# Optimization experiments

Hardware: AMD Instinct MI355X
Metric: run time of the kernel (lower is better)

The kernel has to match this reference:

```python
import jax, jax.numpy as jnp
import numpy as np

B, C, S, D = 16, 32, 64, 512
DFF, E = 2048, 8


def setup_inputs() -> dict:
    key = jax.random.key(0)
    ks = jax.random.split(key, 16)
    std = 0.02
    return {
        'x': jax.random.normal(ks[0], (B, C, S, D), jnp.float32),
        'baseline': jax.random.normal(ks[1], (B, C, S, D), jnp.float32),
        'attnres': jax.random.normal(ks[2], (B, C, S, D), jnp.float32),
        'shared_w1': jax.random.normal(ks[3], (DFF, D), jnp.float32) * std,
        'shared_b1': jnp.zeros((DFF,), jnp.float32),
        'shared_w2': jax.random.normal(ks[4], (D, DFF), jnp.float32) * std,
        'shared_b2': jnp.zeros((D,), jnp.float32),
        'spa_router_w': jax.random.normal(ks[5], (E, 3 * D), jnp.float32) * std,
        'spa_router_b': jnp.zeros((E,), jnp.float32),
        'spe_router_w': jax.random.normal(ks[6], (E, 3 * D), jnp.float32) * std,
        'spe_router_b': jnp.zeros((E,), jnp.float32),
        'spa_w1': jax.random.normal(ks[7], (E, DFF, D), jnp.float32) * std,
        'spa_b1': jnp.zeros((E, DFF), jnp.float32),
        'spa_w2': jax.random.normal(ks[8], (E, D, DFF), jnp.float32) * std,
        'spa_b2': jnp.zeros((E, D), jnp.float32),
        'spe_w1': jax.random.normal(ks[9], (E, DFF, D), jnp.float32) * std,
        'spe_b1': jnp.zeros((E, DFF), jnp.float32),
        'spe_w2': jax.random.normal(ks[10], (E, D, DFF), jnp.float32) * std,
        'spe_b2': jnp.zeros((E, D), jnp.float32),
    }


def _route(feat, rw, rb):
    # feat [B, 3D] -> top-1 expert index [B] and its softmax gate weight [B]
    logits = feat @ rw.T + rb            # [B, E]
    p = jax.nn.softmax(logits, axis=-1)
    idx = jnp.argmax(logits, axis=-1)    # [B]
    w = jnp.take_along_axis(p, idx[:, None], axis=-1)[:, 0]
    return idx, w


def _specialist(xf, idx, w1, b1, w2, b2):
    # xf [B, T, D]; per-sample gather of expert weights then batched FFN
    W1, B1 = w1[idx], b1[idx]            # [B, DFF, D], [B, DFF]
    W2, B2 = w2[idx], b2[idx]            # [B, D, DFF], [B, D]
    h = jax.nn.gelu(jnp.einsum('btd,bfd->btf', xf, W1) + B1[:, None, :])
    return jnp.einsum('btf,bdf->btd', h, W2) + B2[:, None, :]


def reference(x, baseline, attnres, shared_w1, shared_b1, shared_w2, shared_b2,
              spa_router_w, spa_router_b, spe_router_w, spe_router_b,
              spa_w1, spa_b1, spa_w2, spa_b2, spe_w1, spe_b1, spe_w2, spe_b2):
    b, d = x.shape[0], x.shape[-1]
    xf = x.reshape(b, -1, d)  # [B, T, D]
    # sample-level AttnRes router features: [B, 3*d_model]
    feat = jnp.concatenate([
        baseline.mean(axis=(1, 2)),
        attnres.mean(axis=(1, 2)),
        (attnres - baseline).mean(axis=(1, 2)),
    ], axis=-1)
    spa_idx, spa_w = _route(feat, spa_router_w, spa_router_b)
    spe_idx, spe_w = _route(feat, spe_router_w, spe_router_b)
    # shared dense FFN (dropout=0 eval)
    shared = jax.nn.gelu(xf @ shared_w1.T + shared_b1) @ shared_w2.T + shared_b2
    spa_out = _specialist(xf, spa_idx, spa_w1, spa_b1, spa_w2, spa_b2)
    spe_out = _specialist(xf, spe_idx, spe_w1, spe_b1, spe_w2, spe_b2)
    y = shared + spa_w[:, None, None] * spa_out + spe_w[:, None, None] * spe_out
    return y.reshape(x.shape)
```

## Files before the change

### kernel.cpp

```cpp
#include <hip/hip_runtime.h>
#include <cstdint>
#include <cstddef>

#define DEV __device__ __forceinline__

typedef unsigned short u16;
typedef _Float16 f16x8 __attribute__((ext_vector_type(8)));
typedef float f32x4 __attribute__((ext_vector_type(4)));

static constexpr int NB  = 16;
static constexpr int T   = 2048;
static constexpr int D   = 512;
static constexpr int DFF = 2048;
static constexpr int NE  = 8;
static constexpr int FEAT = 3 * D;

#define MFMA16 __builtin_amdgcn_mfma_f32_16x16x32_f16

DEV u16 f2h(float f) {
  _Float16 h = (_Float16)f;
  union { _Float16 h; u16 u; } cv; cv.h = h; return cv.u;
}

DEV float gelu_fast(float x) {
  const float t = x * x;
  const float p = x * fmaf(t, -0.07135481627f, -1.59576912161f);
  return __fdividef(x, 1.0f + __expf(p));
}


__global__ void k_part(const float* __restrict__ base, const float* __restrict__ attn,
                       float* __restrict__ part) {
  const int b = blockIdx.x >> 4, ch = blockIdx.x & 15;
  const int d = threadIdx.x;
  const size_t o = ((size_t)b * T + (size_t)ch * 128) * D + d;
  const float* pb = base + o;
  const float* pa = attn + o;
  float sb = 0.f, sa = 0.f;
  for (int r = 0; r < 128; ++r) { sb += pb[(size_t)r * D]; sa += pa[(size_t)r * D]; }
  part[(b * 16 + ch) * D + d] = sb;
  part[NB * 16 * D + (b * 16 + ch) * D + d] = sa;
}

__global__ void k_feat(const float* __restrict__ part, float* __restrict__ feat) {
  const int b = blockIdx.x, d = threadIdx.x;
  float sb = 0.f, sa = 0.f;
  for (int ch = 0; ch < 16; ++ch) {
    sb += part[(b * 16 + ch) * D + d];
    sa += part[NB * 16 * D + (b * 16 + ch) * D + d];
  }
  sb *= (1.0f / 2048.0f); sa *= (1.0f / 2048.0f);
  feat[b * FEAT + d] = sb;
  feat[b * FEAT + D + d] = sa;
  feat[b * FEAT + 2 * D + d] = sa - sb;
}

__global__ void k_zero(int* __restrict__ used) {
  used[threadIdx.x] = 0;
}

__global__ void k_route(const float* __restrict__ feat,
                        const float* __restrict__ rw0, const float* __restrict__ rb0,
                        const float* __restrict__ rw1, const float* __restrict__ rb1,
                        int* __restrict__ idx, float* __restrict__ gate,
                        int* __restrict__ used) {
  const int r = blockIdx.x >> 4, b = blockIdx.x & 15;
  const float* rw = (r == 0) ? rw0 : rw1;
  const float* rb = (r == 0) ? rb0 : rb1;
  const int l = threadIdx.x;
  float p[8];
#pragma unroll
  for (int e = 0; e < 8; ++e) p[e] = 0.f;
  const float* f = feat + b * FEAT;
  for (int k = l; k < FEAT; k += 64) {
    const float fv = f[k];
#pragma unroll
    for (int e = 0; e < 8; ++e) p[e] += fv * rw[e * FEAT + k];
  }
#pragma unroll
  for (int off = 32; off >= 1; off >>= 1) {
#pragma unroll
    for (int e = 0; e < 8; ++e) p[e] += __shfl_xor(p[e], off);
  }
  if (l == 0) {
    float best = -1e30f; int bi = 0;
    float lg[8];
#pragma unroll
    for (int e = 0; e < 8; ++e) {
      lg[e] = p[e] + rb[e];
      if (lg[e] > best) { best = lg[e]; bi = e; }
    }
    float s = 0.f;
#pragma unroll
    for (int e = 0; e < 8; ++e) s += expf(lg[e] - best);
    idx[r * 16 + b] = bi;
    gate[r * 16 + b] = 1.0f / s;
    atomicOr(&used[r * 8 + bi], 1);
  }
}

__global__ void k_btot(const float* __restrict__ b2s, const float* __restrict__ b2a,
                       const float* __restrict__ b2e, const int* __restrict__ idx,
                       const float* __restrict__ gate, float* __restrict__ btot) {
  const int b = blockIdx.x, d = threadIdx.x;
  const int ia = idx[b], ie = idx[16 + b];
  const float ga = gate[b], ge = gate[16 + b];
  btot[b * D + d] = b2s[d] + ga * b2a[ia * D + d] + ge * b2e[ie * D + d];
}

__global__ void k_cast(const float* __restrict__ s, u16* __restrict__ d, long n) {
  const long i = ((long)blockIdx.x * blockDim.x + threadIdx.x) * 4;
  if (i >= n) return;
  const float4 v = *(const float4*)(s + i);
  const unsigned int lo = (unsigned int)f2h(v.x) | ((unsigned int)f2h(v.y) << 16);
  const unsigned int hi = (unsigned int)f2h(v.z) | ((unsigned int)f2h(v.w) << 16);
  *(uint2*)(d + i) = make_uint2(lo, hi);
}

__global__ void k_cast_gated(const float* __restrict__ s, u16* __restrict__ d,
                             const int* __restrict__ used) {
  const int e = blockIdx.x >> 10;
  if (!used[e]) return;
  const long i = (long)e * (DFF * D) + ((long)(blockIdx.x & 1023) * 256 + threadIdx.x) * 4;
  const float4 v = *(const float4*)(s + i);
  const unsigned int lo = (unsigned int)f2h(v.x) | ((unsigned int)f2h(v.y) << 16);
  const unsigned int hi = (unsigned int)f2h(v.z) | ((unsigned int)f2h(v.w) << 16);
  *(uint2*)(d + i) = make_uint2(lo, hi);
}


DEV void ld_lds16(const void* g, void* l) {
  __builtin_amdgcn_global_load_lds((const __attribute__((address_space(1))) void*)g,
                                   (__attribute__((address_space(3))) void*)l, 16, 0, 0);
}

template <int NC>
DEV void gemm_pipe(const u16* __restrict__ A, int lda, const u16* __restrict__ B, int ldb,
                   u16* As, u16* Bs, f32x4 (&acc)[8][4]) {
  static_assert(NC >= 4 && (NC % 2) == 0, "NC must be even and >= 4");
  const int tid = threadIdx.x;
  const int lane = tid & 63, wid = tid >> 6;
  const int wr = wid >> 2, wc = wid & 3;

  const int r0 = wid * 32 + (lane >> 2);
  const int r1 = r0 + 16;
  const int cb0 = (lane & 3) ^ ((r0 >> 1) & 3);
  const int cb1 = (lane & 3) ^ ((r1 >> 1) & 3);
  const int ldsO0 = wid * 1024;
  const int ldsO1 = wid * 1024 + 512;
  const u16* pA0 = A + (size_t)r0 * lda + cb0 * 8;
  const u16* pA1 = A + (size_t)r1 * lda + cb1 * 8;
  const u16* pB0 = B + (size_t)r0 * ldb + cb0 * 8;
  const u16* pB1 = B + (size_t)r1 * ldb + cb1 * 8;

  const int kb = lane >> 4;
  int ar[8], br[4];
#pragma unroll
  for (int m = 0; m < 8; ++m) {
    const int R = wr * 128 + m * 16 + (lane & 15);
    ar[m] = R * 64 + ((kb ^ ((R >> 1) & 3)) * 16);
  }
#pragma unroll
  for (int n = 0; n < 4; ++n) {
    const int C = wc * 64 + n * 16 + (lane & 15);
    br[n] = C * 64 + ((kb ^ ((C >> 1) & 3)) * 16);
  }

#define STAGE(c) do { const int sl_ = (c) & 3; const long off_ = (long)(c) * 32;   \
    ld_lds16(pA0 + off_, As + sl_ * 8192 + ldsO0);                                 \
    ld_lds16(pA1 + off_, As + sl_ * 8192 + ldsO1);                                 \
    ld_lds16(pB0 + off_, Bs + sl_ * 8192 + ldsO0);                                 \
    ld_lds16(pB1 + off_, Bs + sl_ * 8192 + ldsO1); } while (0)

#define RD_A(dst, c) do { const char* sl_ = (const char*)(As + ((c) & 3) * 8192);  \
    _Pragma("unroll") for (int m_ = 0; m_ < 8; ++m_)                               \
      dst[m_] = *(const f16x8*)(sl_ + ar[m_]); } while (0)

#define RD_B(c) do { const char* sl_ = (const char*)(Bs + ((c) & 3) * 8192);       \
    _Pragma("unroll") for (int n_ = 0; n_ < 4; ++n_)                               \
      bv[n_] = *(const f16x8*)(sl_ + br[n_]); } while (0)

#define MFMA_SET(av) do {                                                          \
    __builtin_amdgcn_s_setprio(1);                                                 \
    _Pragma("unroll") for (int m_ = 0; m_ < 8; ++m_) {                             \
      acc[m_][0] = MFMA16(av[0 + m_], bv[0], acc[m_][0], 0, 0, 0);                 \
      acc[m_][1] = MFMA16(av[0 + m_], bv[1], acc[m_][1], 0, 0, 0);                 \
      acc[m_][2] = MFMA16(av[0 + m_], bv[2], acc[m_][2], 0, 0, 0);                 \
      acc[m_][3] = MFMA16(av[0 + m_], bv[3], acc[m_][3], 0, 0, 0); }               \
    __builtin_amdgcn_s_setprio(0); } while (0)

  f16x8 avA[8], avB[8], bv[4];

  STAGE(0); STAGE(1); STAGE(2);
  asm volatile("s_waitcnt vmcnt(4)" ::: "memory");
  __builtin_amdgcn_s_barrier();
  RD_A(avA, 0);
  RD_B(0);

  for (int c = 0; c < NC; c += 2) {
    {
      RD_A(avB, c + 1);
      if (c + 3 < NC) STAGE(c + 3);
      asm volatile("s_waitcnt lgkmcnt(8)" ::: "memory");
      MFMA_SET(avA);
      RD_B(c + 1);
      if (c + 3 < NC)      asm volatile("s_waitcnt vmcnt(4)" ::: "memory");
      else if (c + 2 < NC) asm volatile("s_waitcnt vmcnt(0)" ::: "memory");
      __builtin_amdgcn_s_barrier();
    }
    {
      const int c1 = c + 1;
      const bool more = (c1 + 1) < NC;
      if (more) RD_A(avA, c1 + 1);
      if (c1 + 3 < NC) STAGE(c1 + 3);
      if (more) asm volatile("s_waitcnt lgkmcnt(8)" ::: "memory");
      else      asm volatile("s_waitcnt lgkmcnt(0)" ::: "memory");
      MFMA_SET(avB);
      if (more) RD_B(c1 + 1);
      if (c1 + 3 < NC)      asm volatile("s_waitcnt vmcnt(4)" ::: "memory");
      else if (c1 + 2 < NC) asm volatile("s_waitcnt vmcnt(0)" ::: "memory");
      __builtin_amdgcn_s_barrier();
    }
  }
#undef STAGE
#undef RD_A
#undef RD_B
#undef MFMA_SET
}

template <int BANK>
__global__ __launch_bounds__(512) void k_ffn1(
    const u16* __restrict__ xh, const u16* __restrict__ w1, const float* __restrict__ b1,
    const int* __restrict__ idx, const float* __restrict__ gate, u16* __restrict__ h) {
  __shared__ alignas(16) u16 As[4 * 8192];
  __shared__ alignas(16) u16 Bs[4 * 8192];
  int wg = blockIdx.x;
  const int q = (int)gridDim.x >> 3;
  wg = (wg & 7) * q + (wg >> 3);
  const int b  = wg >> 6;
  const int mt = (wg >> 3) & 7;
  const int nt = wg & 7;

  const int e   = (BANK == 0) ? 0 : idx[(BANK - 1) * 16 + b];
  const float g = (BANK == 0) ? 1.0f : gate[(BANK - 1) * 16 + b];
  const u16* Ab = xh + ((size_t)b * T + (size_t)mt * 256) * D;
  const u16* Bb = w1 + (size_t)e * DFF * D + (size_t)nt * 256 * D;
  const float* bb = b1 + (size_t)e * DFF;

  f32x4 acc[8][4];
#pragma unroll
  for (int m = 0; m < 8; ++m)
#pragma unroll
    for (int n = 0; n < 4; ++n)
#pragma unroll
      for (int r = 0; r < 4; ++r) acc[m][n][r] = 0.f;

  gemm_pipe<16>(Ab, D, Bb, D, As, Bs, acc);

  const int lane = threadIdx.x & 63, wid = threadIdx.x >> 6;
  const int wr = wid >> 2, wc = wid & 3;
  const int rr = (lane >> 4) << 2, cc = lane & 15;
  const int mrow = mt * 256 + wr * 128;
  const int ncol = nt * 256 + wc * 64;
  u16* hb = h + (size_t)b * T * DFF;
  float bias[4];
#pragma unroll
  for (int n = 0; n < 4; ++n) bias[n] = bb[ncol + n * 16 + cc];
#pragma unroll
  for (int m = 0; m < 8; ++m) {
    const int row = mrow + m * 16 + rr;
#pragma unroll
    for (int n = 0; n < 4; ++n) {
      const int col = ncol + n * 16 + cc;
      const f32x4 a = acc[m][n];
#pragma unroll
      for (int r = 0; r < 4; ++r) {
        const float v = gelu_fast(a[r] + bias[n]) * g;
        hb[(size_t)(row + r) * DFF + col] = f2h(v);
      }
    }
  }
}

template <int BANK>
__global__ __launch_bounds__(512) void k_ffn2(
    const u16* __restrict__ h, const u16* __restrict__ w2, const float* __restrict__ btot,
    const int* __restrict__ idx, float* __restrict__ out) {
  __shared__ alignas(16) u16 As[4 * 8192];
  __shared__ alignas(16) u16 Bs[4 * 8192];
  int wg = blockIdx.x;
  const int q = (int)gridDim.x >> 3;
  wg = (wg & 7) * q + (wg >> 3);
  const int b  = wg >> 4;
  const int mt = (wg >> 1) & 7;
  const int nt = wg & 1;

  const int e = (BANK == 0) ? 0 : idx[(BANK - 1) * 16 + b];
  const u16* Ab = h + ((size_t)b * T + (size_t)mt * 256) * DFF;
  const u16* Bb = w2 + (size_t)e * D * DFF + (size_t)nt * 256 * DFF;

  f32x4 acc[8][4];
#pragma unroll
  for (int m = 0; m < 8; ++m)
#pragma unroll
    for (int n = 0; n < 4; ++n)
#pragma unroll
      for (int r = 0; r < 4; ++r) acc[m][n][r] = 0.f;

  gemm_pipe<64>(Ab, DFF, Bb, DFF, As, Bs, acc);

  const int lane = threadIdx.x & 63, wid = threadIdx.x >> 6;
  const int wr = wid >> 2, wc = wid & 3;
  const int rr = (lane >> 4) << 2, cc = lane & 15;
  const int mrow = mt * 256 + wr * 128;
  const int ncol = nt * 256 + wc * 64;
  float* ob = out + (size_t)b * T * D;
  float bt[4];
#pragma unroll
  for (int n = 0; n < 4; ++n) bt[n] = btot[b * D + ncol + n * 16 + cc];
#pragma unroll
  for (int m = 0; m < 8; ++m) {
    const int row = mrow + m * 16 + rr;
#pragma unroll
    for (int n = 0; n < 4; ++n) {
      const int col = ncol + n * 16 + cc;
      const f32x4 a = acc[m][n];
#pragma unroll
      for (int r = 0; r < 4; ++r) {
        const size_t oi = (size_t)(row + r) * D + col;
        if (BANK == 0) ob[oi] = a[r] + bt[n];
        else           ob[oi] += a[r];
      }
    }
  }
}


extern "C" void kernel_launch(void* const* d_in, const int* in_sizes, int n_in,
                              void* d_out, int out_size, void* d_ws, size_t ws_size,
                              hipStream_t stream) {
  (void)in_sizes; (void)n_in; (void)out_size; (void)ws_size;
  const float* x    = (const float*)d_in[0];
  const float* base = (const float*)d_in[1];
  const float* attn = (const float*)d_in[2];
  const float* sw1  = (const float*)d_in[3];
  const float* sb1  = (const float*)d_in[4];
  const float* sw2  = (const float*)d_in[5];
  const float* sb2  = (const float*)d_in[6];
  const float* arw  = (const float*)d_in[7];
  const float* arb  = (const float*)d_in[8];
  const float* erw  = (const float*)d_in[9];
  const float* erb  = (const float*)d_in[10];
  const float* aw1  = (const float*)d_in[11];
  const float* ab1  = (const float*)d_in[12];
  const float* aw2  = (const float*)d_in[13];
  const float* ab2  = (const float*)d_in[14];
  const float* ew1  = (const float*)d_in[15];
  const float* eb1  = (const float*)d_in[16];
  const float* ew2  = (const float*)d_in[17];
  const float* eb2  = (const float*)d_in[18];
  float* out = (float*)d_out;

  char* w = (char*)d_ws;
  u16* xh   = (u16*)w;  w += (size_t)NB * T * D * 2;
  u16* hbuf = (u16*)w;  w += (size_t)NB * T * DFF * 2;
  u16* w1s  = (u16*)w;  w += (size_t)DFF * D * 2;
  u16* w2s  = (u16*)w;  w += (size_t)D * DFF * 2;
  u16* w1a  = (u16*)w;  w += (size_t)NE * DFF * D * 2;
  u16* w2a  = (u16*)w;  w += (size_t)NE * D * DFF * 2;
  u16* w1e  = (u16*)w;  w += (size_t)NE * DFF * D * 2;
  u16* w2e  = (u16*)w;  w += (size_t)NE * D * DFF * 2;
  float* part = (float*)w; w += (size_t)2 * NB * 16 * D * 4;
  float* feat = (float*)w; w += (size_t)NB * FEAT * 4;
  int*   idx  = (int*)w;   w += 32 * 4;
  float* gate = (float*)w; w += 32 * 4;
  float* btot = (float*)w; w += (size_t)NB * D * 4;
  int*   used = (int*)w;   w += 16 * 4;

  k_zero<<<dim3(1), dim3(16), 0, stream>>>(used);
  k_part<<<dim3(256), dim3(512), 0, stream>>>(base, attn, part);
  k_feat<<<dim3(16), dim3(512), 0, stream>>>(part, feat);
  k_route<<<dim3(32), dim3(64), 0, stream>>>(feat, arw, arb, erw, erb, idx, gate, used);
  k_btot<<<dim3(16), dim3(512), 0, stream>>>(sb2, ab2, eb2, idx, gate, btot);

  {
    long n;
    n = (long)NB * T * D;  k_cast<<<(unsigned)(n / 1024), 256, 0, stream>>>(x,   xh,  n);
    n = (long)DFF * D;     k_cast<<<(unsigned)(n / 1024), 256, 0, stream>>>(sw1, w1s, n);
    n = (long)D * DFF;     k_cast<<<(unsigned)(n / 1024), 256, 0, stream>>>(sw2, w2s, n);
    k_cast_gated<<<dim3(8192), 256, 0, stream>>>(aw1, w1a, used);
    k_cast_gated<<<dim3(8192), 256, 0, stream>>>(aw2, w2a, used);
    k_cast_gated<<<dim3(8192), 256, 0, stream>>>(ew1, w1e, used + 8);
    k_cast_gated<<<dim3(8192), 256, 0, stream>>>(ew2, w2e, used + 8);
  }

  const dim3 g1(1024), g2(256), blk(512);
  k_ffn1<0><<<g1, blk, 0, stream>>>(xh, w1s, sb1, idx, gate, hbuf);
  k_ffn2<0><<<g2, blk, 0, stream>>>(hbuf, w2s, btot, idx, out);
  k_ffn1<1><<<g1, blk, 0, stream>>>(xh, w1a, ab1, idx, gate, hbuf);
  k_ffn2<1><<<g2, blk, 0, stream>>>(hbuf, w2a, btot, idx, out);
  k_ffn1<2><<<g1, blk, 0, stream>>>(xh, w1e, eb1, idx, gate, hbuf);
  k_ffn2<2><<<g2, blk, 0, stream>>>(hbuf, w2e, btot, idx, out);
}
```

Baseline: 753.1 us.

## Replace GEMM mainloop with 8-phase double-buffered K=64 pipeline

Replaces the 4-slot K=32 software pipeline with a 2-slot double buffer of K=64 tiles. Each tile is split into four MFMA quadrants, with LDS reads and global-to-LDS staging interleaved between barrier-separated phases. The aim is better overlap of memory traffic with MFMA work and fewer iterations. In exchange it adds more barriers and lgkmcnt(0) waits per tile, which could serialise execution.

```diff
diff --git a/kernel.cpp b/kernel.cpp
--- a/kernel.cpp
+++ b/kernel.cpp
@@ -134,106 +134,111 @@
                                    (__attribute__((address_space(3))) void*)l, 16, 0, 0);
 }
 
-template <int NC>
-DEV void gemm_pipe(const u16* __restrict__ A, int lda, const u16* __restrict__ B, int ldb,
-                   u16* As, u16* Bs, f32x4 (&acc)[8][4]) {
-  static_assert(NC >= 4 && (NC % 2) == 0, "NC must be even and >= 4");
+#define BAR __builtin_amdgcn_s_barrier()
+#define LGKM0 do { asm volatile("s_waitcnt lgkmcnt(0)" ::: "memory"); \
+                   __builtin_amdgcn_sched_barrier(0); } while (0)
+#define VMW2 asm volatile("s_waitcnt vmcnt(2)" ::: "memory")
+#define VMW0 asm volatile("s_waitcnt vmcnt(0)" ::: "memory")
+
+#define STG_A(tt, h, sb) do { const long ko_ = (long)(tt) * 64;                          \
+    ld_lds16(((h) ? gA10 : gA00) + ko_, (char*)As + (sb) * 32768 + (h) * 16384 + dR0);   \
+    ld_lds16(((h) ? gA11 : gA01) + ko_, (char*)As + (sb) * 32768 + (h) * 16384 + dR1); } while (0)
+#define STG_B(tt, h, sb) do { const long ko_ = (long)(tt) * 64;                          \
+    ld_lds16(((h) ? gB10 : gB00) + ko_, (char*)Bs + (sb) * 32768 + (h) * 16384 + dR0);   \
+    ld_lds16(((h) ? gB11 : gB01) + ko_, (char*)Bs + (sb) * 32768 + (h) * 16384 + dR1); } while (0)
+
+#define RD_A(dst, mb, sb) do {                                                           \
+    _Pragma("unroll") for (int m_ = 0; m_ < 4; ++m_)                                     \
+      _Pragma("unroll") for (int k_ = 0; k_ < 2; ++k_)                                   \
+        dst[m_][k_] = *(const f16x8*)((const char*)As + (sb) * 32768 + avb[k_] +         \
+                                      ((mb) + m_) * 2048); } while (0)
+#define RD_B(dst, nb, sb) do {                                                           \
+    _Pragma("unroll") for (int n_ = 0; n_ < 2; ++n_)                                     \
+      _Pragma("unroll") for (int k_ = 0; k_ < 2; ++k_)                                   \
+        dst[n_][k_] = *(const f16x8*)((const char*)Bs + (sb) * 32768 + bvb[k_] +         \
+                                      ((nb) + n_) * 2048); } while (0)
+
+#define QUAD(av, bv, mb, nb) do { __builtin_amdgcn_s_setprio(1);                         \
+    _Pragma("unroll") for (int m_ = 0; m_ < 4; ++m_)                                     \
+      _Pragma("unroll") for (int n_ = 0; n_ < 2; ++n_) {                                 \
+        acc[(mb)+m_][(nb)+n_] = MFMA16(av[m_][0], bv[n_][0], acc[(mb)+m_][(nb)+n_],0,0,0); \
+        acc[(mb)+m_][(nb)+n_] = MFMA16(av[m_][1], bv[n_][1], acc[(mb)+m_][(nb)+n_],0,0,0); \
+      }                                                                                  \
+    __builtin_amdgcn_s_setprio(0); } while (0)
+
+#define TILE(tt, sb, STGN, STGA0, VMN) do {                                              \
+                                                             \
+    RD_A(avLO, 0, sb); RD_B(bvA, 0, sb);                                                 \
+    if (STGN) { STG_A((tt)+1, 1, (sb)^1); STG_B((tt)+1, 0, (sb)^1); STG_B((tt)+1, 1, (sb)^1); } \
+    BAR; LGKM0; QUAD(avLO, bvA, 0, 0); BAR;                                              \
+                                                             \
+    RD_B(bvB, 2, sb);                                                                    \
+    BAR; LGKM0; QUAD(avLO, bvB, 0, 2); BAR;                                              \
+                                                             \
+    RD_A(avHI, 4, sb);                                                                   \
+    BAR; LGKM0; QUAD(avHI, bvB, 4, 2); BAR;                                              \
+                                                             \
+    RD_B(bvA, 0, sb);                                                                    \
+    if (STGA0) STG_A((tt)+2, 0, sb);                                                     \
+    BAR; LGKM0; QUAD(avHI, bvA, 4, 0);                                                   \
+    if ((VMN) == 2) VMW2; else if ((VMN) == 0) VMW0;                                     \
+    BAR;                                                                                 \
+  } while (0)
+
+template <int NT>
+DEV void gemm_8p(const u16* __restrict__ A, int lda, const u16* __restrict__ B, int ldb,
+                 u16* As, u16* Bs, f32x4 (&acc)[8][4]) {
+  static_assert(NT >= 6 && (NT % 2) == 0, "NT must be even and >= 6");
   const int tid = threadIdx.x;
   const int lane = tid & 63, wid = tid >> 6;
   const int wr = wid >> 2, wc = wid & 3;
 
-  const int r0 = wid * 32 + (lane >> 2);
-  const int r1 = r0 + 16;
-  const int cb0 = (lane & 3) ^ ((r0 >> 1) & 3);
-  const int cb1 = (lane & 3) ^ ((r1 >> 1) & 3);
-  const int ldsO0 = wid * 1024;
-  const int ldsO1 = wid * 1024 + 512;
-  const u16* pA0 = A + (size_t)r0 * lda + cb0 * 8;
-  const u16* pA1 = A + (size_t)r1 * lda + cb1 * 8;
-  const u16* pB0 = B + (size_t)r0 * ldb + cb0 * 8;
-  const u16* pB1 = B + (size_t)r1 * ldb + cb1 * 8;
-
-  const int kb = lane >> 4;
-  int ar[8], br[4];
-#pragma unroll
-  for (int m = 0; m < 8; ++m) {
-    const int R = wr * 128 + m * 16 + (lane & 15);
-    ar[m] = R * 64 + ((kb ^ ((R >> 1) & 3)) * 16);
-  }
-#pragma unroll
-  for (int n = 0; n < 4; ++n) {
-    const int C = wc * 64 + n * 16 + (lane & 15);
-    br[n] = C * 64 + ((kb ^ ((C >> 1) & 3)) * 16);
-  }
-
-#define STAGE(c) do { const int sl_ = (c) & 3; const long off_ = (long)(c) * 32;   \
-    ld_lds16(pA0 + off_, As + sl_ * 8192 + ldsO0);                                 \
-    ld_lds16(pA1 + off_, As + sl_ * 8192 + ldsO1);                                 \
-    ld_lds16(pB0 + off_, Bs + sl_ * 8192 + ldsO0);                                 \
-    ld_lds16(pB1 + off_, Bs + sl_ * 8192 + ldsO1); } while (0)
-
-#define RD_A(dst, c) do { const char* sl_ = (const char*)(As + ((c) & 3) * 8192);  \
-    _Pragma("unroll") for (int m_ = 0; m_ < 8; ++m_)                               \
-      dst[m_] = *(const f16x8*)(sl_ + ar[m_]); } while (0)
-
-#define RD_B(c) do { const char* sl_ = (const char*)(Bs + ((c) & 3) * 8192);       \
-    _Pragma("unroll") for (int n_ = 0; n_ < 4; ++n_)                               \
-      bv[n_] = *(const f16x8*)(sl_ + br[n_]); } while (0)
-
-#define MFMA_SET(av) do {                                                          \
-    __builtin_amdgcn_s_setprio(1);                                                 \
-    _Pragma("unroll") for (int m_ = 0; m_ < 8; ++m_) {                             \
-      acc[m_][0] = MFMA16(av[0 + m_], bv[0], acc[m_][0], 0, 0, 0);                 \
-      acc[m_][1] = MFMA16(av[0 + m_], bv[1], acc[m_][1], 0, 0, 0);                 \
-      acc[m_][2] = MFMA16(av[0 + m_], bv[2], acc[m_][2], 0, 0, 0);                 \
-      acc[m_][3] = MFMA16(av[0 + m_], bv[3], acc[m_][3], 0, 0, 0); }               \
-    __builtin_amdgcn_s_setprio(0); } while (0)
-
-  f16x8 avA[8], avB[8], bv[4];
-
-  STAGE(0); STAGE(1); STAGE(2);
-  asm volatile("s_waitcnt vmcnt(4)" ::: "memory");
-  __builtin_amdgcn_s_barrier();
-  RD_A(avA, 0);
-  RD_B(0);
-
-  for (int c = 0; c < NC; c += 2) {
-    {
-      RD_A(avB, c + 1);
-      if (c + 3 < NC) STAGE(c + 3);
-      asm volatile("s_waitcnt lgkmcnt(8)" ::: "memory");
-      MFMA_SET(avA);
-      RD_B(c + 1);
-      if (c + 3 < NC)      asm volatile("s_waitcnt vmcnt(4)" ::: "memory");
-      else if (c + 2 < NC) asm volatile("s_waitcnt vmcnt(0)" ::: "memory");
-      __builtin_amdgcn_s_barrier();
-    }
-    {
-      const int c1 = c + 1;
-      const bool more = (c1 + 1) < NC;
-      if (more) RD_A(avA, c1 + 1);
-      if (c1 + 3 < NC) STAGE(c1 + 3);
-      if (more) asm volatile("s_waitcnt lgkmcnt(8)" ::: "memory");
-      else      asm volatile("s_waitcnt lgkmcnt(0)" ::: "memory");
-      MFMA_SET(avB);
-      if (more) RD_B(c1 + 1);
-      if (c1 + 3 < NC)      asm volatile("s_waitcnt vmcnt(4)" ::: "memory");
-      else if (c1 + 2 < NC) asm volatile("s_waitcnt vmcnt(0)" ::: "memory");
-      __builtin_amdgcn_s_barrier();
-    }
-  }
-#undef STAGE
-#undef RD_A
-#undef RD_B
-#undef MFMA_SET
+  const int srow = lane >> 3;
+  const int scol = (lane & 7) ^ srow;
+  const int rj0 = wid * 16 + srow;
+  const int rj1 = rj0 + 8;
+  const u16* gA00 = A + (size_t)(  0 + rj0) * lda + scol * 8;
+  const u16* gA01 = A + (size_t)(  0 + rj1) * lda + scol * 8;
+  const u16* gA10 = A + (size_t)(128 + rj0) * lda + scol * 8;
+  const u16* gA11 = A + (size_t)(128 + rj1) * lda + scol * 8;
+  const u16* gB00 = B + (size_t)(  0 + rj0) * ldb + scol * 8;
+  const u16* gB01 = B + (size_t)(  0 + rj1) * ldb + scol * 8;
+  const u16* gB10 = B + (size_t)(128 + rj0) * ldb + scol * 8;
+  const u16* gB11 = B + (size_t)(128 + rj1) * ldb + scol * 8;
+  const int dR0 = (wid * 16) * 128;
+  const int dR1 = dR0 + 1024;
+
+  const int aR = wr * 128 + (lane & 15);
+  const int bR = wc * 64 + (lane & 15);
+  const int sH = lane >> 4;
+  int avb[2], bvb[2];
+#pragma unroll
+  for (int k_ = 0; k_ < 2; ++k_) {
+    const int s_ = (k_ * 4 + sH);
+    avb[k_] = aR * 128 + ((s_ ^ (lane & 7)) * 16);
+    bvb[k_] = bR * 128 + ((s_ ^ (lane & 7)) * 16);
+  }
+
+  f16x8 avLO[4][2], avHI[4][2], bvA[2][2], bvB[2][2];
+
+  STG_A(0, 0, 0); STG_A(0, 1, 0); STG_B(0, 0, 0); STG_B(0, 1, 0);
+  STG_A(1, 0, 1);
+  VMW2; BAR;
+
+  for (int tp = 0; tp < (NT - 2) / 2; ++tp) {
+    TILE(2 * tp,     0, true, true, 2);
+    TILE(2 * tp + 1, 1, true, true, 2);
+  }
+  TILE(NT - 2, 0, true,  false, 0);
+  TILE(NT - 1, 1, false, false, -1);
 }
 
 template <int BANK>
 __global__ __launch_bounds__(512) void k_ffn1(
     const u16* __restrict__ xh, const u16* __restrict__ w1, const float* __restrict__ b1,
     const int* __restrict__ idx, const float* __restrict__ gate, u16* __restrict__ h) {
-  __shared__ alignas(16) u16 As[4 * 8192];
-  __shared__ alignas(16) u16 Bs[4 * 8192];
+  __shared__ alignas(16) u16 As[2 * 16384];
+  __shared__ alignas(16) u16 Bs[2 * 16384];
   int wg = blockIdx.x;
   const int q = (int)gridDim.x >> 3;
   wg = (wg & 7) * q + (wg >> 3);
@@ -255,7 +260,7 @@
 #pragma unroll
       for (int r = 0; r < 4; ++r) acc[m][n][r] = 0.f;
 
-  gemm_pipe<16>(Ab, D, Bb, D, As, Bs, acc);
+  gemm_8p<8>(Ab, D, Bb, D, As, Bs, acc);
 
   const int lane = threadIdx.x & 63, wid = threadIdx.x >> 6;
   const int wr = wid >> 2, wc = wid & 3;
@@ -286,8 +291,8 @@
 __global__ __launch_bounds__(512) void k_ffn2(
     const u16* __restrict__ h, const u16* __restrict__ w2, const float* __restrict__ btot,
     const int* __restrict__ idx, float* __restrict__ out) {
-  __shared__ alignas(16) u16 As[4 * 8192];
-  __shared__ alignas(16) u16 Bs[4 * 8192];
+  __shared__ alignas(16) u16 As[2 * 16384];
+  __shared__ alignas(16) u16 Bs[2 * 16384];
   int wg = blockIdx.x;
   const int q = (int)gridDim.x >> 3;
   wg = (wg & 7) * q + (wg >> 3);
@@ -307,7 +312,7 @@
 #pragma unroll
       for (int r = 0; r < 4; ++r) acc[m][n][r] = 0.f;
 
-  gemm_pipe<64>(Ab, DFF, Bb, DFF, As, Bs, acc);
+  gemm_8p<32>(Ab, DFF, Bb, DFF, As, Bs, acc);
 
   const int lane = threadIdx.x & 63, wid = threadIdx.x >> 6;
   const int wr = wid >> 2, wc = wid & 3;
@@ -315,9 +320,10 @@
   const int mrow = mt * 256 + wr * 128;
   const int ncol = nt * 256 + wc * 64;
   float* ob = out + (size_t)b * T * D;
-  float bt[4];
-#pragma unroll
-  for (int n = 0; n < 4; ++n) bt[n] = btot[b * D + ncol + n * 16 + cc];
+  const float* bt = btot + b * D;
+  float btv[4];
+#pragma unroll
+  for (int n = 0; n < 4; ++n) btv[n] = bt[ncol + n * 16 + cc];
 #pragma unroll
   for (int m = 0; m < 8; ++m) {
     const int row = mrow + m * 16 + rr;
@@ -328,7 +334,7 @@
 #pragma unroll
       for (int r = 0; r < 4; ++r) {
         const size_t oi = (size_t)(row + r) * D + col;
-        if (BANK == 0) ob[oi] = a[r] + bt[n];
+        if (BANK == 0) ob[oi] = a[r] + btv[n];
         else           ob[oi] += a[r];
       }
     }
```

New measurement: 727.9 us. 1.03x faster.
